# Optimization experiments

Measured on AMD Instinct MI355X. Metric: run time of the kernel, lower is better.

## Reference

```python
import jax, jax.numpy as jnp
import numpy as np

BITS = 8
QMAX = float(2 ** (BITS - 1) - 1)   # 127
QMIN = -float(2 ** (BITS - 1))      # -128
LORA_SCALING = 2.0                  # alpha=16 / r=8


def fake_quant(x):
    """Per-tensor symmetric fake quantization with STE (STE irrelevant for fwd)."""
    scale = jnp.maximum(jnp.max(jnp.abs(x)) / QMAX, 1e-8)
    y = jnp.clip(jnp.round(x / scale), QMIN, QMAX) * scale
    return x + jax.lax.stop_gradient(y - x)


def qat_linear_lora(x, W, b, A, B):
    # fake-quantized main path + full-precision LoRA path
    xq = fake_quant(x)
    Wq = fake_quant(W)
    main = jnp.einsum('bsi,oi->bso', xq, Wq) + b
    lora = jnp.einsum('bsr,or->bso', jnp.einsum('bsi,ri->bsr', x, A), B) * LORA_SCALING
    return main + lora


def setup_inputs() -> dict:
    key = jax.random.key(0)
    ks = jax.random.split(key, 6)
    n_embd, d_ff, r = 1024, 4096, 8
    B_, S = 4, 2048
    return {
        'hidden_states': jax.random.normal(ks[0], (B_, S, n_embd), jnp.float32),
        'W_fc': jax.random.normal(ks[1], (d_ff, n_embd), jnp.float32) * 0.02,
        'b_fc': jnp.zeros((d_ff,), jnp.float32),
        'A_fc': jax.random.normal(ks[2], (r, n_embd), jnp.float32) * (1.0 / n_embd) ** 0.5,
        'B_fc': jnp.zeros((d_ff, r), jnp.float32),
        'W_proj': jax.random.normal(ks[3], (n_embd, d_ff), jnp.float32) * 0.02,
        'b_proj': jnp.zeros((n_embd,), jnp.float32),
        'A_proj': jax.random.normal(ks[4], (r, d_ff), jnp.float32) * (1.0 / d_ff) ** 0.5,
        'B_proj': jnp.zeros((n_embd, r), jnp.float32),
    }


def reference(hidden_states, W_fc, b_fc, A_fc, B_fc, W_proj, b_proj, A_proj, B_proj):
    h = qat_linear_lora(hidden_states, W_fc, b_fc, A_fc, B_fc)
    h = jax.nn.gelu(h, approximate=False)  # nn.GELU() default = exact erf GELU
    h = qat_linear_lora(h, W_proj, b_proj, A_proj, B_proj)
    return h
```

## Files before the change

### kernel.cpp

```cpp
#include <hip/hip_runtime.h>
#include <hip/hip_bf16.h>
#include <hip/hip_fp16.h>
#include <math.h>


typedef unsigned short u16;
typedef unsigned int u32;
typedef signed char i8;
typedef int i32x4 __attribute__((ext_vector_type(4)));
typedef _Float16 f16;
typedef f16 f16x8 __attribute__((ext_vector_type(8)));
typedef float f32x4 __attribute__((ext_vector_type(4)));

#define ASYNC16(gp, lp)                                                        \
  __builtin_amdgcn_global_load_lds(                                            \
      (__attribute__((address_space(1))) void*)(gp),                           \
      (__attribute__((address_space(3))) void*)(lp), 16, 0, 0)

__device__ __forceinline__ int quanti(float v, float inv) {
  float q = rintf(v * inv);
  q = fminf(fmaxf(q, -128.0f), 127.0f);
  return (int)q;
}

__device__ __forceinline__ float load_scale(const u32* slot) {
  return fmaxf(__uint_as_float(*slot) * (1.0f / 127.0f), 1e-8f);
}

__device__ __forceinline__ float gelu_erf(float v) {
  float z = fabsf(v) * 0.70710678118654752f;
  float t = __builtin_amdgcn_rcpf(fmaf(0.3275911f, z, 1.0f));
  float poly =
      t * fmaf(t,
               fmaf(t,
                    fmaf(t, fmaf(t, 1.061405429f, -1.453152027f),
                         1.421413741f),
                    -0.284496736f),
               0.254829592f);
  float e = fmaf(-poly, exp2f(-z * z * 1.4426950408889634f), 1.0f);
  return 0.5f * v * fmaf(copysignf(e, v), 1.0f, 1.0f);
}

__global__ void absmax_kernel(const float* __restrict__ x, int n4,
                              u32* __restrict__ slot) {
  float m = 0.0f;
  int stride = gridDim.x * blockDim.x;
  for (int i = blockIdx.x * blockDim.x + threadIdx.x; i < n4; i += stride) {
    float4 v = ((const float4*)x)[i];
    m = fmaxf(m, fmaxf(fmaxf(fabsf(v.x), fabsf(v.y)),
                       fmaxf(fabsf(v.z), fabsf(v.w))));
  }
#pragma unroll
  for (int off = 32; off > 0; off >>= 1) m = fmaxf(m, __shfl_down(m, off));
  __shared__ float wmax[4];
  int lane = threadIdx.x & 63, wave = threadIdx.x >> 6;
  if (lane == 0) wmax[wave] = m;
  __syncthreads();
  if (threadIdx.x == 0) {
    m = fmaxf(fmaxf(wmax[0], wmax[1]), fmaxf(wmax[2], wmax[3]));
    atomicMax(slot, __float_as_uint(m));
  }
}

__global__ void quant_w_kernel(const float* __restrict__ w, int n16,
                               const u32* __restrict__ slot,
                               i8* __restrict__ q) {
  float inv = 1.0f / load_scale(slot);
  int stride = gridDim.x * blockDim.x;
  for (int i = blockIdx.x * blockDim.x + threadIdx.x; i < n16; i += stride) {
    const float4* src = (const float4*)w + i * 4;
    u32 pk[4];
#pragma unroll
    for (int c = 0; c < 4; c++) {
      float4 v = src[c];
      pk[c] = ((u32)(quanti(v.x, inv) & 255)) |
              ((u32)(quanti(v.y, inv) & 255) << 8) |
              ((u32)(quanti(v.z, inv) & 255) << 16) |
              ((u32)(quanti(v.w, inv) & 255) << 24);
    }
    uint4 o = {pk[0], pk[1], pk[2], pk[3]};
    ((uint4*)q)[i] = o;
  }
}

__global__ void quant_x_t1_kernel(const float* __restrict__ x,
                                  const float* __restrict__ A,
                                  const u32* __restrict__ slot,
                                  i8* __restrict__ q,
                                  float* __restrict__ t1) {
  int row = blockIdx.x, tid = threadIdx.x;
  float inv = 1.0f / load_scale(slot);
  float4 v = ((const float4*)(x + (long)row * 1024))[tid];
  u32 pk = ((u32)(quanti(v.x, inv) & 255)) |
           ((u32)(quanti(v.y, inv) & 255) << 8) |
           ((u32)(quanti(v.z, inv) & 255) << 16) |
           ((u32)(quanti(v.w, inv) & 255) << 24);
  ((u32*)(q + (long)row * 1024))[tid] = pk;
  float p[8];
#pragma unroll
  for (int r = 0; r < 8; r++) {
    float4 a = ((const float4*)(A + r * 1024))[tid];
    p[r] = v.x * a.x + v.y * a.y + v.z * a.z + v.w * a.w;
  }
#pragma unroll
  for (int r = 0; r < 8; r++)
#pragma unroll
    for (int off = 32; off > 0; off >>= 1) p[r] += __shfl_down(p[r], off);
  __shared__ float red[4][8];
  int lane = tid & 63, wave = tid >> 6;
  if (lane == 0) {
#pragma unroll
    for (int r = 0; r < 8; r++) red[wave][r] = p[r];
  }
  __syncthreads();
  if (tid < 8)
    t1[(long)row * 8 + tid] =
        red[0][tid] + red[1][tid] + red[2][tid] + red[3][tid];
}

__global__ void conv_a16_kernel(const float* __restrict__ A,
                                f16* __restrict__ Ah) {
  int i = blockIdx.x * blockDim.x + threadIdx.x;
  int base = i * 8;
  if (base < 8 * 4096) {
    float4 v0 = ((const float4*)(A + base))[0];
    float4 v1 = ((const float4*)(A + base))[1];
    f16x8 o = {(f16)v0.x, (f16)v0.y, (f16)v0.z, (f16)v0.w,
               (f16)v1.x, (f16)v1.y, (f16)v1.z, (f16)v1.w};
    *(f16x8*)(Ah + base) = o;
  } else {
    f16x8 z = {};
    *(f16x8*)(Ah + base) = z;
  }
}

__launch_bounds__(256) __global__
    void quant_h_t2_fused(u16* __restrict__ h,
                          const f16* __restrict__ Ah,
                          const u32* __restrict__ slot,
                          float* __restrict__ t2) {
  int tid = threadIdx.x;
  int lane = tid & 63, wave = tid >> 6;
  int quad = lane >> 4, l15 = lane & 15;
  int bx = blockIdx.x;
  long m0 = (long)blockIdx.y * 64 + wave * 16;
  long row = m0 + l15;
  int k0 = bx * 512;
  float inv = 1.0f / load_scale(slot);

  const u16* hp = h + row * 4096 + k0 + quad * 8;
  const f16* ap = Ah + l15 * 4096 + k0 + quad * 8;
  f32x4 acc = {0.0f, 0.0f, 0.0f, 0.0f};
  u32 q[32];
#pragma unroll
  for (int s = 0; s < 16; s++) {
    uint4 hv = *(const uint4*)(hp + s * 32);
    f16x8 af = *(const f16x8*)&hv;
    f16x8 bf = *(const f16x8*)(ap + s * 32);
    acc = __builtin_amdgcn_mfma_f32_16x16x32_f16(af, bf, acc, 0, 0, 0);
    u32 uu[4] = {hv.x, hv.y, hv.z, hv.w};
#pragma unroll
    for (int c = 0; c < 2; c++) {
      float2 f0 = __half22float2(*(__half2*)&uu[2 * c]);
      float2 f1 = __half22float2(*(__half2*)&uu[2 * c + 1]);
      q[2 * s + c] = ((u32)(quanti(f0.x, inv) & 255)) |
                     ((u32)(quanti(f0.y, inv) & 255) << 8) |
                     ((u32)(quanti(f1.x, inv) & 255) << 16) |
                     ((u32)(quanti(f1.y, inv) & 255) << 24);
    }
  }
  asm volatile("" ::: "memory");
  i8* op = (i8*)h + row * 8192 + bx * 1024 + quad * 8;
#pragma unroll
  for (int s = 0; s < 16; s++) {
    uint2 o = {q[2 * s], q[2 * s + 1]};
    *(uint2*)(op + s * 32) = o;
  }
  if (l15 < 8) {
#pragma unroll
    for (int r = 0; r < 4; r++) {
      long m = m0 + quad * 4 + r;
      atomicAdd(&t2[m * 8 + l15], acc[r]);
    }
  }
}

template <int MODE>
__launch_bounds__(256) __global__
    void gemm_kernel(const i8* __restrict__ A, const i8* __restrict__ B,
                     int N, int K, int lda, int ldb,
                     const float* __restrict__ bias,
                     const float* __restrict__ tl,
                     const float* __restrict__ Bl,
                     const u32* __restrict__ scales, int sa, int sb,
                     void* __restrict__ outp, u32* __restrict__ hmax) {
  __shared__ i8 As[128 * 128];
  __shared__ i8 Bs[128 * 128];
  __shared__ u32 bmax;
  int tid = threadIdx.x;
  int lane = tid & 63, wave = tid >> 6;
  int quad = lane >> 4, l15 = lane & 15;
  int wm = (wave & 1) * 64, wn = (wave >> 1) * 64;
  long m0 = (long)blockIdx.y * 128;
  long n0 = (long)blockIdx.x * 128;
  if (MODE == 0 && tid == 0) bmax = 0u;

  const i8* gA[4];
  const i8* gB[4];
  int ldsOff[4];
#pragma unroll
  for (int i = 0; i < 4; i++) {
    int c = i * 256 + tid;
    int row = c >> 3;
    int kc = ((c & 7) ^ (row & 7)) * 16;
    gA[i] = A + (m0 + row) * lda + kc;
    gB[i] = B + (n0 + row) * ldb + kc;
    ldsOff[i] = c * 16;
  }
  int s0 = (quad ^ (l15 & 7)) * 16;
  int s1 = s0 ^ 64;

  i32x4 acc[4][4] = {};
  int nit = K >> 7;
  for (int k = 0; k < nit; k++) {
    int adv = (MODE == 1 && (k & 3) == 3) ? 640 : 128;
#pragma unroll
    for (int i = 0; i < 4; i++) {
      ASYNC16(gA[i], As + ldsOff[i]);
      ASYNC16(gB[i], Bs + ldsOff[i]);
      gA[i] += adv;
      gB[i] += 128;
    }
    __syncthreads();
#pragma unroll
    for (int kk = 0; kk < 2; kk++) {
      int ko = kk ? s1 : s0;
      i32x4 af[4], bfr[4];
#pragma unroll
      for (int i = 0; i < 4; i++)
        af[i] = *(const i32x4*)(As + (wm + i * 16 + l15) * 128 + ko);
#pragma unroll
      for (int j = 0; j < 4; j++)
        bfr[j] = *(const i32x4*)(Bs + (wn + j * 16 + l15) * 128 + ko);
#pragma unroll
      for (int i = 0; i < 4; i++)
#pragma unroll
        for (int j = 0; j < 4; j++)
          acc[i][j] = __builtin_amdgcn_mfma_i32_16x16x64_i8(
              af[i], bfr[j], acc[i][j], 0, 0, 0);
    }
    __syncthreads();
  }

  float scale = load_scale(scales + sa) * load_scale(scales + sb);
  float biasv[4];
  float4 bl0[4], bl1[4];
#pragma unroll
  for (int j = 0; j < 4; j++) {
    long n = n0 + wn + j * 16 + l15;
    biasv[j] = bias[n];
    bl0[j] = ((const float4*)(Bl + n * 8))[0];
    bl1[j] = ((const float4*)(Bl + n * 8))[1];
  }
  float lmax = 0.0f;
#pragma unroll
  for (int i = 0; i < 4; i++) {
#pragma unroll
    for (int r = 0; r < 4; r++) {
      long m = m0 + wm + i * 16 + quad * 4 + r;
      float4 t0 = ((const float4*)(tl + m * 8))[0];
      float4 t1v = ((const float4*)(tl + m * 8))[1];
#pragma unroll
      for (int j = 0; j < 4; j++) {
        long n = n0 + wn + j * 16 + l15;
        float lora = t0.x * bl0[j].x + t0.y * bl0[j].y + t0.z * bl0[j].z +
                     t0.w * bl0[j].w + t1v.x * bl1[j].x + t1v.y * bl1[j].y +
                     t1v.z * bl1[j].z + t1v.w * bl1[j].w;
        float v = (float)acc[i][j][r] * scale + biasv[j] + 2.0f * lora;
        if (MODE == 0) {
          float hv = gelu_erf(v);
          __half hh = __float2half_rn(hv);
          ((u16*)outp)[m * N + n] = *(u16*)&hh;
          lmax = fmaxf(lmax, fabsf(hv));
        } else {
          ((float*)outp)[m * N + n] = v;
        }
      }
    }
  }
  if (MODE == 0) {
    atomicMax(&bmax, __float_as_uint(lmax));
    __syncthreads();
    if (tid == 0) atomicMax(hmax, bmax);
  }
}

extern "C" void kernel_launch(void* const* d_in, const int* in_sizes, int n_in,
                              void* d_out, int out_size, void* d_ws,
                              size_t ws_size, hipStream_t stream) {
  const float* x = (const float*)d_in[0];
  const float* Wfc = (const float*)d_in[1];
  const float* bfc = (const float*)d_in[2];
  const float* Afc = (const float*)d_in[3];
  const float* Bfc = (const float*)d_in[4];
  const float* Wpr = (const float*)d_in[5];
  const float* bpr = (const float*)d_in[6];
  const float* Apr = (const float*)d_in[7];
  const float* Bpr = (const float*)d_in[8];
  float* out = (float*)d_out;

  char* w = (char*)d_ws;
  u32* scales = (u32*)w;
  float* t1 = (float*)(w + 256);
  float* t2 = (float*)(w + 256 + 262144);
  i8* xq = (i8*)(w + 524544);
  f16* aprh = (f16*)(w + 8913152);
  i8* wq1 = (i8*)(w + 9437184);
  i8* wq2 = (i8*)(w + 13631488);
  u16* hq = (u16*)(w + 17825792);
  if (ws_size < 84934656) return;

  hipMemsetAsync(scales, 0, 256, stream);
  hipMemsetAsync(t2, 0, 262144, stream);
  conv_a16_kernel<<<64, 256, 0, stream>>>(Apr, aprh);
  absmax_kernel<<<1024, 256, 0, stream>>>(x, 8192 * 1024 / 4, scales + 0);
  absmax_kernel<<<512, 256, 0, stream>>>(Wfc, 4096 * 1024 / 4, scales + 1);
  absmax_kernel<<<512, 256, 0, stream>>>(Wpr, 4096 * 1024 / 4, scales + 2);
  quant_x_t1_kernel<<<8192, 256, 0, stream>>>(x, Afc, scales + 0, xq, t1);
  quant_w_kernel<<<256, 256, 0, stream>>>(Wfc, 4096 * 1024 / 16, scales + 1,
                                          wq1);
  quant_w_kernel<<<256, 256, 0, stream>>>(Wpr, 4096 * 1024 / 16, scales + 2,
                                          wq2);
  gemm_kernel<0><<<dim3(32, 64), 256, 0, stream>>>(
      xq, wq1, 4096, 1024, 1024, 1024, bfc, t1, Bfc, scales, 0, 1, hq,
      scales + 3);
  quant_h_t2_fused<<<dim3(8, 128), 256, 0, stream>>>(hq, aprh, scales + 3, t2);
  gemm_kernel<1><<<dim3(8, 64), 256, 0, stream>>>(
      (const i8*)hq, wq2, 1024, 4096, 8192, 4096, bpr, t2, Bpr, scales, 3, 2,
      out, nullptr);
}
```

Baseline: 329.0 us.

## Rewrite int8 GEMMs as 8-wave double-buffered pipelined kernels with larger tiles

Replaces the single-buffer 128x128 int8 GEMM with a 512-thread kernel using 256xBN tiles and double-buffered LDS. Async global-to-LDS loads for the next tiles are interleaved with MFMA phases using explicit vmcnt/lgkmcnt waits, barriers and setprio. It also adds an XCD-aware block swizzle. The goal is to hide global load latency and raise data reuse per block. The cost is much larger LDS use (up to 128KB per block), which limits occupancy, and fragile manual wait counts.

Result: faster. 320.9 us (-2.5%).

```diff
diff --git a/kernel.cpp b/kernel.cpp
--- a/kernel.cpp
+++ b/kernel.cpp
@@ -16,6 +16,14 @@
   __builtin_amdgcn_global_load_lds(                                            \
       (__attribute__((address_space(1))) void*)(gp),                           \
       (__attribute__((address_space(3))) void*)(lp), 16, 0, 0)
+
+#define VMCNT(N) asm volatile("s_waitcnt vmcnt(" #N ")" ::: "memory")
+#define LGKM0                                                                  \
+  do {                                                                         \
+    asm volatile("s_waitcnt lgkmcnt(0)" ::: "memory");                         \
+    __builtin_amdgcn_sched_barrier(0);                                         \
+  } while (0)
+#define SBAR __builtin_amdgcn_s_barrier()
 
 __device__ __forceinline__ int quanti(float v, float inv) {
   float q = rintf(v * inv);
@@ -185,78 +193,159 @@
   }
 }
 
-template <int MODE>
-__launch_bounds__(256) __global__
-    void gemm_kernel(const i8* __restrict__ A, const i8* __restrict__ B,
-                     int N, int K, int lda, int ldb,
-                     const float* __restrict__ bias,
-                     const float* __restrict__ tl,
-                     const float* __restrict__ Bl,
-                     const u32* __restrict__ scales, int sa, int sb,
-                     void* __restrict__ outp, u32* __restrict__ hmax) {
-  __shared__ i8 As[128 * 128];
-  __shared__ i8 Bs[128 * 128];
+template <int MODE, int BN, int WARPS_M>
+__launch_bounds__(512, 2) __global__
+    void gemm8p_kernel(const i8* __restrict__ A, const i8* __restrict__ B,
+                       int N, int K, int lda, int ldb,
+                       const float* __restrict__ bias,
+                       const float* __restrict__ tl,
+                       const float* __restrict__ Bl,
+                       const u32* __restrict__ scales, int sa, int sb,
+                       void* __restrict__ outp, u32* __restrict__ hmax) {
+  constexpr int WARPS_N = 8 / WARPS_M;
+  constexpr int MT = 256 / (16 * WARPS_M);
+  constexpr int NT = BN / (16 * WARPS_N);
+  constexpr int LB = BN / 128;
+  __shared__ __align__(16) i8 As[2][256 * 128];
+  __shared__ __align__(16) i8 Bs[2][BN * 128];
   __shared__ u32 bmax;
   int tid = threadIdx.x;
   int lane = tid & 63, wave = tid >> 6;
   int quad = lane >> 4, l15 = lane & 15;
-  int wm = (wave & 1) * 64, wn = (wave >> 1) * 64;
-  long m0 = (long)blockIdx.y * 128;
-  long n0 = (long)blockIdx.x * 128;
+  int wm = (wave % WARPS_M) * (MT * 16);
+  int wn = (wave / WARPS_M) * (NT * 16);
+  int nwg = gridDim.x * gridDim.y;
+  int lin = blockIdx.y * gridDim.x + blockIdx.x;
+  int swb = (lin & 7) * (nwg >> 3) + (lin >> 3);
+  int bx = swb % gridDim.x, by = swb / gridDim.x;
+  long m0 = (long)by * 256;
+  long n0 = (long)bx * BN;
   if (MODE == 0 && tid == 0) bmax = 0u;
 
-  const i8* gA[4];
-  const i8* gB[4];
-  int ldsOff[4];
-#pragma unroll
-  for (int i = 0; i < 4; i++) {
-    int c = i * 256 + tid;
+  const i8* pA[2];
+  int ldsA[2];
+#pragma unroll
+  for (int u = 0; u < 2; u++) {
+    int c = u * 512 + tid;
     int row = c >> 3;
-    int kc = ((c & 7) ^ (row & 7)) * 16;
-    gA[i] = A + (m0 + row) * lda + kc;
-    gB[i] = B + (n0 + row) * ldb + kc;
-    ldsOff[i] = c * 16;
-  }
+    int swz = ((c & 7) ^ (row & 7)) * 16;
+    pA[u] = A + (m0 + row) * lda + swz;
+    ldsA[u] = c * 16;
+  }
+  const i8* pB[LB];
+  int ldsB[LB];
+#pragma unroll
+  for (int u = 0; u < LB; u++) {
+    int c = u * 512 + tid;
+    int row = c >> 3;
+    int swz = ((c & 7) ^ (row & 7)) * 16;
+    pB[u] = B + (n0 + row) * ldb + swz;
+    ldsB[u] = c * 16;
+  }
+
+  auto stageA = [&](int t, int h) {
+    int kb = (MODE == 1) ? ((t >> 2) * 1024 + (t & 3) * 128) : (t << 7);
+    int bb = t & 1;
+#pragma unroll
+    for (int u = 0; u < 2; u++)
+      ASYNC16(pA[u] + (long)h * 128 * lda + kb,
+              &As[bb][h * 16384 + ldsA[u]]);
+  };
+  auto stageB = [&](int t, int h) {
+    int kb = t << 7;
+    int bb = t & 1;
+#pragma unroll
+    for (int u = 0; u < LB; u++)
+      ASYNC16(pB[u] + (long)h * (BN / 2) * ldb + kb,
+              &Bs[bb][h * (BN / 2) * 128 + ldsB[u]]);
+  };
+
   int s0 = (quad ^ (l15 & 7)) * 16;
   int s1 = s0 ^ 64;
 
-  i32x4 acc[4][4] = {};
-  int nit = K >> 7;
-  for (int k = 0; k < nit; k++) {
-    int adv = (MODE == 1 && (k & 3) == 3) ? 640 : 128;
-#pragma unroll
-    for (int i = 0; i < 4; i++) {
-      ASYNC16(gA[i], As + ldsOff[i]);
-      ASYNC16(gB[i], Bs + ldsOff[i]);
-      gA[i] += adv;
-      gB[i] += 128;
+  i32x4 acc[MT][NT] = {};
+  int NTILES = K >> 7;
+
+  stageA(0, 0); stageA(0, 1); stageB(0, 0); stageB(0, 1);
+  stageA(1, 0); stageA(1, 1);
+  VMCNT(4);
+  SBAR;
+
+  for (int t = 0; t < NTILES; t++) {
+    const i8* Ab = As[t & 1];
+    const i8* Bb = Bs[t & 1];
+    i32x4 a0[MT], a1[MT], b0[NT], b1[NT];
+#pragma unroll
+    for (int i = 0; i < MT; i++)
+      a0[i] = *(const i32x4*)(Ab + (wm + i * 16 + l15) * 128 + s0);
+#pragma unroll
+    for (int j = 0; j < NT; j++)
+      b0[j] = *(const i32x4*)(Bb + (wn + j * 16 + l15) * 128 + s0);
+    if (t + 1 < NTILES) stageB(t + 1, 0);
+    SBAR;
+    LGKM0;
+    __builtin_amdgcn_s_setprio(1);
+#pragma unroll
+    for (int i = 0; i < MT / 2; i++)
+#pragma unroll
+      for (int j = 0; j < NT; j++)
+        acc[i][j] = __builtin_amdgcn_mfma_i32_16x16x64_i8(a0[i], b0[j],
+                                                          acc[i][j], 0, 0, 0);
+    __builtin_amdgcn_s_setprio(0);
+    SBAR;
+#pragma unroll
+    for (int i = 0; i < MT; i++)
+      a1[i] = *(const i32x4*)(Ab + (wm + i * 16 + l15) * 128 + s1);
+    if (t + 1 < NTILES) stageB(t + 1, 1);
+    SBAR;
+    LGKM0;
+    __builtin_amdgcn_s_setprio(1);
+#pragma unroll
+    for (int i = MT / 2; i < MT; i++)
+#pragma unroll
+      for (int j = 0; j < NT; j++)
+        acc[i][j] = __builtin_amdgcn_mfma_i32_16x16x64_i8(a0[i], b0[j],
+                                                          acc[i][j], 0, 0, 0);
+    __builtin_amdgcn_s_setprio(0);
+    SBAR;
+#pragma unroll
+    for (int j = 0; j < NT; j++)
+      b1[j] = *(const i32x4*)(Bb + (wn + j * 16 + l15) * 128 + s1);
+    if (t + 2 < NTILES) stageA(t + 2, 0);
+    SBAR;
+    LGKM0;
+    __builtin_amdgcn_s_setprio(1);
+#pragma unroll
+    for (int i = 0; i < MT / 2; i++)
+#pragma unroll
+      for (int j = 0; j < NT; j++)
+        acc[i][j] = __builtin_amdgcn_mfma_i32_16x16x64_i8(a1[i], b1[j],
+                                                          acc[i][j], 0, 0, 0);
+    __builtin_amdgcn_s_setprio(0);
+    SBAR;
+    if (t + 2 < NTILES) stageA(t + 2, 1);
+    SBAR;
+    __builtin_amdgcn_s_setprio(1);
+#pragma unroll
+    for (int i = MT / 2; i < MT; i++)
+#pragma unroll
+      for (int j = 0; j < NT; j++)
+        acc[i][j] = __builtin_amdgcn_mfma_i32_16x16x64_i8(a1[i], b1[j],
+                                                          acc[i][j], 0, 0, 0);
+    __builtin_amdgcn_s_setprio(0);
+    if (t + 2 < NTILES) {
+      VMCNT(4);
+    } else {
+      VMCNT(0);
     }
-    __syncthreads();
-#pragma unroll
-    for (int kk = 0; kk < 2; kk++) {
-      int ko = kk ? s1 : s0;
-      i32x4 af[4], bfr[4];
-#pragma unroll
-      for (int i = 0; i < 4; i++)
-        af[i] = *(const i32x4*)(As + (wm + i * 16 + l15) * 128 + ko);
-#pragma unroll
-      for (int j = 0; j < 4; j++)
-        bfr[j] = *(const i32x4*)(Bs + (wn + j * 16 + l15) * 128 + ko);
-#pragma unroll
-      for (int i = 0; i < 4; i++)
-#pragma unroll
-        for (int j = 0; j < 4; j++)
-          acc[i][j] = __builtin_amdgcn_mfma_i32_16x16x64_i8(
-              af[i], bfr[j], acc[i][j], 0, 0, 0);
-    }
-    __syncthreads();
+    SBAR;
   }
 
   float scale = load_scale(scales + sa) * load_scale(scales + sb);
-  float biasv[4];
-  float4 bl0[4], bl1[4];
-#pragma unroll
-  for (int j = 0; j < 4; j++) {
+  float biasv[NT];
+  float4 bl0[NT], bl1[NT];
+#pragma unroll
+  for (int j = 0; j < NT; j++) {
     long n = n0 + wn + j * 16 + l15;
     biasv[j] = bias[n];
     bl0[j] = ((const float4*)(Bl + n * 8))[0];
@@ -264,14 +353,14 @@
   }
   float lmax = 0.0f;
 #pragma unroll
-  for (int i = 0; i < 4; i++) {
+  for (int i = 0; i < MT; i++) {
 #pragma unroll
     for (int r = 0; r < 4; r++) {
       long m = m0 + wm + i * 16 + quad * 4 + r;
       float4 t0 = ((const float4*)(tl + m * 8))[0];
       float4 t1v = ((const float4*)(tl + m * 8))[1];
 #pragma unroll
-      for (int j = 0; j < 4; j++) {
+      for (int j = 0; j < NT; j++) {
         long n = n0 + wn + j * 16 + l15;
         float lora = t0.x * bl0[j].x + t0.y * bl0[j].y + t0.z * bl0[j].z +
                      t0.w * bl0[j].w + t1v.x * bl1[j].x + t1v.y * bl1[j].y +
@@ -331,11 +420,11 @@
                                           wq1);
   quant_w_kernel<<<256, 256, 0, stream>>>(Wpr, 4096 * 1024 / 16, scales + 2,
                                           wq2);
-  gemm_kernel<0><<<dim3(32, 64), 256, 0, stream>>>(
+  gemm8p_kernel<0, 256, 2><<<dim3(16, 32), 512, 0, stream>>>(
       xq, wq1, 4096, 1024, 1024, 1024, bfc, t1, Bfc, scales, 0, 1, hq,
       scales + 3);
   quant_h_t2_fused<<<dim3(8, 128), 256, 0, stream>>>(hq, aprh, scales + 3, t2);
-  gemm_kernel<1><<<dim3(8, 64), 256, 0, stream>>>(
+  gemm8p_kernel<1, 128, 4><<<dim3(8, 32), 512, 0, stream>>>(
       (const i8*)hq, wq2, 1024, 4096, 8192, 4096, bpr, t2, Bpr, scales, 3, 2,
       out, nullptr);
 }
```
